# Optimization experiments

Hardware: AMD Instinct MI355X
Metric: run time of the kernel (lower is better)

## Reference

```python
import jax, jax.numpy as jnp
import numpy as np
from jax import lax

N_MAX = 350  # fixed adjacency size from the original module

def _conv(x, w, b):
    y = lax.conv_general_dilated(x, w, (1, 1), 'SAME',
                                 dimension_numbers=('NCHW', 'OIHW', 'NCHW'))
    return y + b[None, :, None, None]

def _maxpool2(x):
    return lax.reduce_window(x, -jnp.inf, lax.max, (1, 1, 2, 2), (1, 1, 2, 2), 'VALID')

def _lin(x, w, b):  # torch Linear: w [out,in]
    return x @ w.T + b

def setup_inputs() -> dict:
    key = jax.random.key(0)
    ks = jax.random.split(key, 24)
    B = 16
    images = jax.random.normal(ks[0], (B, 1, 256, 256), dtype=jnp.float32)
    # prefix masks: first n_b nodes valid, n_b in [2, 350]
    counts = jax.random.randint(ks[1], (B,), 2, N_MAX + 1)
    node_masks = jnp.arange(N_MAX)[None, :] < counts[:, None]
    def p(k, shape, s=0.02):
        return jax.random.normal(k, shape, dtype=jnp.float32) * s
    inp = {
        'images': images, 'node_masks': node_masks,
        # baseline CNN: 1->32->64->128->256, 3x3 convs
        'c1w': p(ks[2], (32, 1, 3, 3)),   'c1b': p(ks[3], (32,)),
        'c2w': p(ks[4], (64, 32, 3, 3)),  'c2b': p(ks[5], (64,)),
        'c3w': p(ks[6], (128, 64, 3, 3)), 'c3b': p(ks[7], (128,)),
        'c4w': p(ks[8], (256, 128, 3, 3)),'c4b': p(ks[9], (256,)),
        # node_detector: 256->512->700
        'nd1w': p(ks[10], (512, 256)), 'nd1b': p(ks[11], (512,)),
        'nd2w': p(ks[12], (N_MAX * 2, 512)), 'nd2b': p(ks[13], (N_MAX * 2,)),
        # count_predictor: 256->256->1
        'cp1w': p(ks[14], (256, 256)), 'cp1b': p(ks[15], (256,)),
        'cp2w': p(ks[16], (1, 256)),   'cp2b': p(ks[17], (1,)),
        # mlp_correction: 1->32->16->1
        'mc1w': p(ks[18], (32, 1)),  'mc1b': p(ks[19], (32,)),
        'mc2w': p(ks[20], (16, 32)), 'mc2b': p(ks[21], (16,)),
        'mc3w': p(ks[22], (1, 16)),  'mc3b': p(ks[23], (1,)),
    }
    return inp

def reference(images, node_masks,
              c1w, c1b, c2w, c2b, c3w, c3b, c4w, c4b,
              nd1w, nd1b, nd2w, nd2b,
              cp1w, cp1b, cp2w, cp2b,
              mc1w, mc1b, mc2w, mc2b, mc3w, mc3b):
    B = images.shape[0]
    relu = jax.nn.relu
    # CNN encoder (baseline)
    x = _maxpool2(relu(_conv(images, c1w, c1b)))
    x = _maxpool2(relu(_conv(x, c2w, c2b)))
    x = _maxpool2(relu(_conv(x, c3w, c3b)))
    x = relu(_conv(x, c4w, c4b))
    feat = jnp.mean(x, axis=(2, 3))  # AdaptiveAvgPool2d((1,1)) -> [B,256]
    # node detector (dropout is identity in eval)
    coords = _lin(relu(_lin(feat, nd1w, nd1b)), nd2w, nd2b).reshape(B, N_MAX, 2)
    # count predictor
    count = _lin(relu(_lin(feat, cp1w, cp1b)), cp2w, cp2b)[:, 0]
    # cosine similarity over all 350 slots (row-wise normalize is mask-independent)
    cn = coords / jnp.maximum(jnp.linalg.norm(coords, axis=-1, keepdims=True), 1e-12)
    sim = jnp.einsum('bnd,bmd->bnm', cn, cn)  # [B,350,350]
    # pointwise 1->32->16->1 MLP correction + sigmoid
    h1 = relu(sim[..., None] * mc1w[:, 0] + mc1b)          # [B,N,N,32]
    h2 = relu(jnp.einsum('bnmk,jk->bnmj', h1, mc2w) + mc2b)  # [B,N,N,16]
    corr = jax.nn.sigmoid(jnp.einsum('bnmj,oj->bnmo', h2, mc3w)[..., 0] + mc3b[0])
    # scatter-pad into fixed 350x350: with prefix masks this is elementwise pair masking
    m = node_masks.astype(corr.dtype)
    pair = m[:, :, None] * m[:, None, :]
    valid = (node_masks.sum(-1) > 1).astype(corr.dtype)  # n_nodes<=1 -> zero adj
    adjacency = corr * pair * valid[:, None, None]
    return (coords, adjacency, count)
```

## Files before the change

kernel.cpp:

```cpp
#include <hip/hip_runtime.h>
#include <hip/hip_bf16.h>
#include <math.h>

typedef __hip_bfloat16 bf16;
typedef __attribute__((ext_vector_type(8))) short short8;
typedef __attribute__((ext_vector_type(4))) float f32x4;

__device__ __forceinline__ bf16 f2b(float v){ return __float2bfloat16(v); }
__device__ __forceinline__ float ldf(float v){ return v; }
__device__ __forceinline__ float ldf(bf16 v){ return __bfloat162float(v); }
__device__ __forceinline__ unsigned short fbits(float v){
  __hip_bfloat16 h = __float2bfloat16(v);
  return *reinterpret_cast<unsigned short*>(&h);
}
__device__ __forceinline__ float dot4(float4 a, float4 b){
  return fmaf(a.x,b.x, fmaf(a.y,b.y, fmaf(a.z,b.z, a.w*b.w)));
}
__device__ __forceinline__ void load_lds16(const bf16* src, void* lds){
  __builtin_amdgcn_global_load_lds(
      (const __attribute__((address_space(1))) void*)src,
      (__attribute__((address_space(3))) void*)lds, 16, 0, 0);
}

__global__ __launch_bounds__(256) void k_c1prep(const float* __restrict__ img,
                        const float* __restrict__ c1w, const float* __restrict__ c1b,
                        bf16* __restrict__ x1,
                        const float* __restrict__ c2w, const float* __restrict__ c3w,
                        const float* __restrict__ c4w, bf16* __restrict__ wt2,
                        bf16* __restrict__ wt3, bf16* __restrict__ wt4,
                        const float* __restrict__ w1, const float* __restrict__ b1,
                        const float* __restrict__ w2, const float* __restrict__ b2,
                        const float* __restrict__ w3, const float* __restrict__ b3,
                        float* __restrict__ lut){
  int bid = blockIdx.x;
  int tid = threadIdx.x;
  if(bid >= 1024){
    int pb = bid - 1024;
    if(pb < 1512){
      int e = pb*256 + tid;
      const float* w; bf16* wt; int OC, IC;
      if(e < 18432){ w = c2w; wt = wt2; OC = 64;  IC = 32; }
      else if(e < 92160){ e -= 18432; w = c3w; wt = wt3; OC = 128; IC = 64; }
      else { e -= 92160; w = c4w; wt = wt4; OC = 256; IC = 128; }
      int ic = e % IC; int t2 = e / IC; int oc = t2 % OC; int tap = t2 / OC;
      wt[e] = f2b(w[(oc*IC + ic)*9 + tap]);
    } else {
      int e = (pb-1512)*256 + tid;
      float s = -1.f + (2.f/4095.f)*e;
      float h1[32];
      #pragma unroll
      for(int k=0;k<32;k++) h1[k] = fmaxf(fmaf(s, w1[k], b1[k]), 0.f);
      float a3 = b3[0];
      #pragma unroll
      for(int j=0;j<16;j++){
        float t = b2[j];
        #pragma unroll
        for(int k=0;k<32;k++) t = fmaf(h1[k], w2[j*32+k], t);
        a3 = fmaf(fmaxf(t,0.f), w3[j], a3);
      }
      lut[e] = 1.f/(1.f + expf(-a3));
    }
    return;
  }
  __shared__ float Wl[288], Bl[32];
  for(int t=tid; t<288; t+=256) Wl[t] = c1w[t];
  if(tid<32) Bl[tid] = c1b[tid];
  __syncthreads();
  int idx = bid*256 + tid;
  int ox = idx & 127, oy = (idx>>7)&127, b = idx>>14;
  const float* ip = img + (size_t)b*65536;
  int y0 = oy*2-1, x0 = ox*2-1;
  float patch[4][4];
  #pragma unroll
  for(int py=0;py<4;py++){
    int y=y0+py; bool yok = (unsigned)y<256u;
    #pragma unroll
    for(int px=0;px<4;px++){
      int x=x0+px;
      patch[py][px] = (yok && (unsigned)x<256u) ? ip[y*256+x] : 0.f;
    }
  }
  unsigned u[16];
  #pragma unroll
  for(int og=0; og<16; og++){
    unsigned short hb[2];
    #pragma unroll
    for(int h=0; h<2; h++){
      int oc = og*2 + h;
      const float* wj = &Wl[oc*9];
      float best = 0.f;
      #pragma unroll
      for(int py=0;py<2;py++)
      #pragma unroll
      for(int px=0;px<2;px++){
        float a = Bl[oc];
        #pragma unroll
        for(int ky=0;ky<3;ky++)
        #pragma unroll
        for(int kx=0;kx<3;kx++)
          a = fmaf(wj[ky*3+kx], patch[py+ky][px+kx], a);
        best = fmaxf(best, a);
      }
      hb[h] = fbits(best);
    }
    u[og] = (unsigned)hb[0] | ((unsigned)hb[1] << 16);
  }
  uint4* dst = (uint4*)(x1 + (size_t)idx*32);
  dst[0] = make_uint4(u[0],u[1],u[2],u[3]);
  dst[1] = make_uint4(u[4],u[5],u[6],u[7]);
  dst[2] = make_uint4(u[8],u[9],u[10],u[11]);
  dst[3] = make_uint4(u[12],u[13],u[14],u[15]);
}

template<int L>
__global__ __launch_bounds__(256) void k_convmfma(const bf16* __restrict__ in,
                      const bf16* __restrict__ wt, const float* __restrict__ bias,
                      bf16* __restrict__ out, float* __restrict__ partial2){
  constexpr int IC   = L==2?32:(L==3?64:128);
  constexpr int OC   = L==2?64:(L==3?128:256);
  constexpr int HW   = L==2?128:(L==3?64:32);
  constexpr int POOL = L==4?0:1;
  constexpr int WNF  = L==4?2:4;
  constexpr int IC8  = IC/8;
  constexpr int SM   = (IC8-1)&7;
  constexpr int KC   = IC/32;
  constexpr int XT   = HW;
  constexpr int ROW  = XT*IC8;
  constexpr int ROWC = (XT+2)*IC8;
  __shared__ short8 T[4*ROWC];

  int bid = blockIdx.x;
  int b, py, bt = 0;
  if(L==4){ b = bid>>5; py = (bid>>1)&15; bt = bid&1; }
  else if(L==3){ b = bid>>5; py = bid&31; }
  else { b = bid>>6; py = bid&63; }

  int tid = threadIdx.x;
  int w = tid>>6, l15 = tid&15, lhi = (tid>>4)&3, lane = tid&63;

  int mbase, nbase;
  if(L==2){ mbase = w*32; nbase = 0; }
  else if(L==3){ mbase = (w&1)*32; nbase = (w>>1)*64; }
  else { mbase = 0; nbase = bt*128 + w*32; }

  for(int c=tid; c<4*2*IC8; c+=256){
    int r = c/(2*IC8), rem = c%(2*IC8);
    int X = (rem>=IC8)?(XT+1):0;
    int k = rem%IC8;
    short8 z = {0,0,0,0,0,0,0,0};
    T[(r*(XT+2)+X)*IC8 + k] = z;
  }
  for(int c0=0; c0<4*ROW; c0+=256){
    int cw  = c0 + w*64;
    int r   = cw / ROW;
    int rem = cw % ROW;
    int gy  = 2*py - 1 + r;
    int ldsbase = (r*(XT+2)+1)*IC8 + rem;
    if((unsigned)gy < (unsigned)HW){
      int remL = rem + lane;
      int x = remL / IC8, k = remL % IC8;
      int ksrc = k ^ ((x+1)&SM);
      const bf16* src = in + (((size_t)b*HW + gy)*XT + x)*IC + ksrc*8;
      load_lds16(src, (void*)&T[ldsbase]);
    } else {
      short8 z = {0,0,0,0,0,0,0,0};
      T[ldsbase + lane] = z;
    }
  }
  __syncthreads();

  float bv[WNF];
  #pragma unroll
  for(int n=0;n<WNF;n++) bv[n] = bias[nbase + n*16 + l15];
  f32x4 acc[2][2][WNF];
  #pragma unroll
  for(int r=0;r<2;r++)
  #pragma unroll
  for(int m=0;m<2;m++)
  #pragma unroll
  for(int n=0;n<WNF;n++){
    acc[r][m][n][0]=bv[n]; acc[r][m][n][1]=bv[n];
    acc[r][m][n][2]=bv[n]; acc[r][m][n][3]=bv[n];
  }

  const short8* wt8 = (const short8*)wt;
  #pragma unroll
  for(int tap=0; tap<9; tap++){
    const int dy = tap/3 - 1, dx = tap%3 - 1;
    #pragma unroll
    for(int kc=0; kc<KC; kc++){
      short8 Bf[WNF];
      #pragma unroll
      for(int n=0;n<WNF;n++){
        int oc = nbase + n*16 + l15;
        Bf[n] = wt8[(size_t)(tap*OC + oc)*IC8 + kc*4 + lhi];
      }
      short8 Af[2][2];
      #pragma unroll
      for(int r=0;r<2;r++)
      #pragma unroll
      for(int m=0;m<2;m++){
        int X = mbase + m*16 + l15 + dx + 1;
        int rs = r + dy + 1;
        Af[r][m] = T[(rs*(XT+2)+X)*IC8 + ((kc*4+lhi) ^ (X&SM))];
      }
      #pragma unroll
      for(int r=0;r<2;r++)
      #pragma unroll
      for(int m=0;m<2;m++)
      #pragma unroll
      for(int n=0;n<WNF;n++)
        acc[r][m][n] = __builtin_amdgcn_mfma_f32_16x16x32_bf16(Af[r][m], Bf[n], acc[r][m][n], 0,0,0);
    }
  }

  if(POOL){
    constexpr int HP = HW/2;
    #pragma unroll
    for(int m=0;m<2;m++)
    #pragma unroll
    for(int n=0;n<WNF;n++){
      int oc = nbase + n*16 + l15;
      #pragma unroll
      for(int t=0;t<2;t++){
        float v = fmaxf(fmaxf(acc[0][m][n][2*t], acc[0][m][n][2*t+1]),
                        fmaxf(acc[1][m][n][2*t], acc[1][m][n][2*t+1]));
        v = fmaxf(v, 0.f);
        int xp = (mbase + m*16)/2 + lhi*2 + t;
        out[(((size_t)b*HP + py)*HP + xp)*OC + oc] = f2b(v);
      }
    }
  } else {
    #pragma unroll
    for(int n=0;n<WNF;n++){
      float p = 0.f;
      #pragma unroll
      for(int r=0;r<2;r++)
      #pragma unroll
      for(int m=0;m<2;m++)
      #pragma unroll
      for(int j=0;j<4;j++)
        p += fmaxf(acc[r][m][n][j], 0.f);
      p += __shfl_xor(p, 16);
      p += __shfl_xor(p, 32);
      if(lhi == 0)
        partial2[((size_t)(b*16+py))*256 + nbase + n*16 + l15] = p;
    }
  }
}

__global__ __launch_bounds__(256) void k_headA(const float* __restrict__ partial2,
                      const float* __restrict__ nd1w, const float* __restrict__ nd1b,
                      const float* __restrict__ cp1w, const float* __restrict__ cp1b,
                      float* __restrict__ h512, float* __restrict__ h256){
  __shared__ float F[256];
  int b = blockIdx.x / 192, blk = blockIdx.x % 192;
  int tid = threadIdx.x;
  float s = 0.f;
  #pragma unroll
  for(int q=0;q<16;q++) s += partial2[((size_t)(b*16+q))*256 + tid];
  F[tid] = s * (1.f/1024.f);
  __syncthreads();
  int w = tid>>6, lane = tid&63;
  int o = blk*4 + w;
  float4 xv = ((const float4*)F)[lane];
  const float* wrow; float bb; float* dst; int oo;
  if(o < 512){ wrow = nd1w + (size_t)o*256; bb = nd1b[o]; dst = h512 + b*512 + o; }
  else { oo = o - 512; wrow = cp1w + (size_t)oo*256; bb = cp1b[oo]; dst = h256 + b*256 + oo; }
  float a = dot4(((const float4*)wrow)[lane], xv);
  #pragma unroll
  for(int off=32; off>0; off>>=1) a += __shfl_xor(a, off);
  if(lane==0) *dst = fmaxf(a + bb, 0.f);
}

__global__ __launch_bounds__(256) void k_headB(const float* __restrict__ h512,
                      const float* __restrict__ h256,
                      const float* __restrict__ nd2w, const float* __restrict__ nd2b,
                      const float* __restrict__ cp2w, const float* __restrict__ cp2b,
                      float* __restrict__ coordsOut, float* __restrict__ countOut){
  int b = blockIdx.x / 176, blk = blockIdx.x % 176;
  int tid = threadIdx.x;
  int w = tid>>6, lane = tid&63;
  int o = blk*4 + w;
  if(o > 700) return;
  float a;
  if(o < 700){
    const float4* xp = (const float4*)(h512 + b*512);
    const float4* wp = (const float4*)(nd2w + (size_t)o*512);
    a = dot4(wp[lane], xp[lane]) + dot4(wp[lane+64], xp[lane+64]);
  } else {
    const float4* xp = (const float4*)(h256 + b*256);
    const float4* wp = (const float4*)cp2w;
    a = dot4(wp[lane], xp[lane]);
  }
  #pragma unroll
  for(int off=32; off>0; off>>=1) a += __shfl_xor(a, off);
  if(lane==0){
    if(o < 700) coordsOut[b*700 + o] = a + nd2b[o];
    else        countOut[b] = a + cp2b[0];
  }
}

__device__ __forceinline__ int mask_mode(const void* p){
  unsigned w0 = ((const unsigned*)p)[0];
  unsigned w1 = ((const unsigned*)p)[1];
  if(w0 == 1u) return (w1 == 0u) ? 4 : 0;
  if(w0 == 0x3F800000u) return 3;
  unsigned short h0 = (unsigned short)(w0 & 0xFFFFu);
  if(h0 == 0x3F80u || h0 == 0x3C00u) return 2;
  return 1;
}
__device__ __forceinline__ int mask_get(const void* p, int i, int mode){
  switch(mode){
    case 0: return ((const int*)p)[i] != 0;
    case 1: return ((const unsigned char*)p)[i] != 0;
    case 2: return ((const unsigned short*)p)[i] != 0;
    case 3: return ((const float*)p)[i] != 0.f;
    default: return ((const long long*)p)[i] != 0ll;
  }
}

__global__ __launch_bounds__(256) void k_adj(const float* __restrict__ coords,
                      const void* __restrict__ masks, const float* __restrict__ lut,
                      float* __restrict__ out){
  int t4 = blockIdx.x*256 + threadIdx.x;
  if(t4 >= 490000) return;
  int base = t4*4;
  int b = base / 122500;
  int rem = base % 122500;
  int mode = mask_mode(masks);
  int valid = mask_get(masks, b*350+1, mode);
  float res[4];
  #pragma unroll
  for(int e=0;e<4;e++){
    int n = (rem+e)/350, m = (rem+e)%350;
    float o = 0.f;
    if(valid && mask_get(masks, b*350+n, mode) && mask_get(masks, b*350+m, mode)){
      float2 a = ((const float2*)coords)[b*350+n];
      float2 c = ((const float2*)coords)[b*350+m];
      float dn = fmaxf(sqrtf(fmaf(a.x,a.x, a.y*a.y)), 1e-12f);
      float dm = fmaxf(sqrtf(fmaf(c.x,c.x, c.y*c.y)), 1e-12f);
      float s = fmaf(a.x, c.x, a.y*c.y) / (dn*dm);
      float u = (s + 1.f) * 2047.5f;
      u = fminf(fmaxf(u, 0.f), 4095.f);
      int i = min((int)u, 4094);
      float fr = u - (float)i;
      float l0 = lut[i], l1 = lut[i+1];
      o = fmaf(l1 - l0, fr, l0);
    }
    res[e] = o;
  }
  *(float4*)(out + base) = make_float4(res[0], res[1], res[2], res[3]);
}

extern "C" void kernel_launch(void* const* d_in, const int* in_sizes, int n_in,
                              void* d_out, int out_size, void* d_ws, size_t ws_size,
                              hipStream_t stream){
  const float* images = (const float*)d_in[0];
  const void*  masks  = d_in[1];
  const float *c1w=(const float*)d_in[2],  *c1b=(const float*)d_in[3];
  const float *c2w=(const float*)d_in[4],  *c2b=(const float*)d_in[5];
  const float *c3w=(const float*)d_in[6],  *c3b=(const float*)d_in[7];
  const float *c4w=(const float*)d_in[8],  *c4b=(const float*)d_in[9];
  const float *nd1w=(const float*)d_in[10],*nd1b=(const float*)d_in[11];
  const float *nd2w=(const float*)d_in[12],*nd2b=(const float*)d_in[13];
  const float *cp1w=(const float*)d_in[14],*cp1b=(const float*)d_in[15];
  const float *cp2w=(const float*)d_in[16],*cp2b=(const float*)d_in[17];
  const float *mc1w=(const float*)d_in[18],*mc1b=(const float*)d_in[19];
  const float *mc2w=(const float*)d_in[20],*mc2b=(const float*)d_in[21];
  const float *mc3w=(const float*)d_in[22],*mc3b=(const float*)d_in[23];
  float* out = (float*)d_out;

  char* W = (char*)d_ws;
  float* partial2 = (float*)W;
  float* h512     = (float*)(W + 262144);
  float* h256     = (float*)(W + 294912);
  float* lut      = (float*)(W + 311296);
  bf16*  wt2 = (bf16*)(W + 524288);
  bf16*  wt3 = (bf16*)(W + 589824);
  bf16*  wt4 = (bf16*)(W + 786432);
  bf16*  x1 = (bf16*)(W + 2097152);
  bf16*  x2 = (bf16*)(W + 2097152 + 16777216);
  bf16*  x3 = (bf16*)(W + 2097152);

  float* coordsOut = out;
  float* adjOut    = out + 11200;
  float* countOut  = out + 11200 + 1960000;

  k_c1prep<<<2552, 256, 0, stream>>>(images, c1w, c1b, x1,
                                     c2w, c3w, c4w, wt2, wt3, wt4,
                                     mc1w, mc1b, mc2w, mc2b, mc3w, mc3b, lut);
  k_convmfma<2><<<1024, 256, 0, stream>>>(x1, wt2, c2b, x2, nullptr);
  k_convmfma<3><<<512, 256, 0, stream>>>(x2, wt3, c3b, x3, nullptr);
  k_convmfma<4><<<512, 256, 0, stream>>>(x3, wt4, c4b, nullptr, partial2);
  k_headA<<<3072, 256, 0, stream>>>(partial2, nd1w, nd1b, cp1w, cp1b, h512, h256);
  k_headB<<<2816, 256, 0, stream>>>(h512, h256, nd2w, nd2b, cp2w, cp2b,
                                    coordsOut, countOut);
  k_adj<<<1915, 256, 0, stream>>>(coordsOut, masks, lut, adjOut);
}
```

Measured before the change: 95.57 us.

## Split conv4 over input channels and precompute mask counts for adjacency

Conv4 is split into two input-channel halves across twice as many blocks, each writing raw per-pixel partial sums to a large workspace. The head kernel then combines the halves, applies ReLU and averages over all pixels. Mask counts are computed once in the second head kernel so the adjacency kernel can use prefix comparisons. The split adds a large global write and a heavy redundant re-read in every head block.

```diff
diff --git a/kernel.cpp b/kernel.cpp
--- a/kernel.cpp
+++ b/kernel.cpp
@@ -122,16 +122,16 @@
   constexpr int POOL = L==4?0:1;
   constexpr int WNF  = L==4?2:4;
   constexpr int IC8  = IC/8;
-  constexpr int SM   = (IC8-1)&7;
-  constexpr int KC   = IC/32;
+  constexpr int IC8S = L==4?8:IC8;
+  constexpr int SMS  = (IC8S-1)&7;
+  constexpr int KCS  = L==4?2:IC/32;
   constexpr int XT   = HW;
-  constexpr int ROW  = XT*IC8;
-  constexpr int ROWC = (XT+2)*IC8;
-  __shared__ short8 T[4*ROWC];
+  constexpr int ROW  = XT*IC8S;
+  __shared__ short8 T[4*(XT+2)*IC8S];
 
   int bid = blockIdx.x;
-  int b, py, bt = 0;
-  if(L==4){ b = bid>>5; py = (bid>>1)&15; bt = bid&1; }
+  int b, py, bt = 0, kq = 0;
+  if(L==4){ b = bid>>6; py = (bid>>2)&15; bt = (bid>>1)&1; kq = bid&1; }
   else if(L==3){ b = bid>>5; py = bid&31; }
   else { b = bid>>6; py = bid&63; }
 
@@ -143,23 +143,23 @@
   else if(L==3){ mbase = (w&1)*32; nbase = (w>>1)*64; }
   else { mbase = 0; nbase = bt*128 + w*32; }
 
-  for(int c=tid; c<4*2*IC8; c+=256){
-    int r = c/(2*IC8), rem = c%(2*IC8);
-    int X = (rem>=IC8)?(XT+1):0;
-    int k = rem%IC8;
+  for(int c=tid; c<4*2*IC8S; c+=256){
+    int r = c/(2*IC8S), rem = c%(2*IC8S);
+    int X = (rem>=IC8S)?(XT+1):0;
+    int k = rem%IC8S;
     short8 z = {0,0,0,0,0,0,0,0};
-    T[(r*(XT+2)+X)*IC8 + k] = z;
+    T[(r*(XT+2)+X)*IC8S + k] = z;
   }
   for(int c0=0; c0<4*ROW; c0+=256){
     int cw  = c0 + w*64;
     int r   = cw / ROW;
     int rem = cw % ROW;
     int gy  = 2*py - 1 + r;
-    int ldsbase = (r*(XT+2)+1)*IC8 + rem;
+    int ldsbase = (r*(XT+2)+1)*IC8S + rem;
     if((unsigned)gy < (unsigned)HW){
       int remL = rem + lane;
-      int x = remL / IC8, k = remL % IC8;
-      int ksrc = k ^ ((x+1)&SM);
+      int x = remL / IC8S, k = remL % IC8S;
+      int ksrc = (k ^ ((x+1)&SMS)) + (L==4 ? kq*8 : 0);
       const bf16* src = in + (((size_t)b*HW + gy)*XT + x)*IC + ksrc*8;
       load_lds16(src, (void*)&T[ldsbase]);
     } else {
@@ -171,7 +171,8 @@
 
   float bv[WNF];
   #pragma unroll
-  for(int n=0;n<WNF;n++) bv[n] = bias[nbase + n*16 + l15];
+  for(int n=0;n<WNF;n++)
+    bv[n] = (L==4 && kq==1) ? 0.f : bias[nbase + n*16 + l15];
   f32x4 acc[2][2][WNF];
   #pragma unroll
   for(int r=0;r<2;r++)
@@ -188,12 +189,12 @@
   for(int tap=0; tap<9; tap++){
     const int dy = tap/3 - 1, dx = tap%3 - 1;
     #pragma unroll
-    for(int kc=0; kc<KC; kc++){
+    for(int kc=0; kc<KCS; kc++){
       short8 Bf[WNF];
       #pragma unroll
       for(int n=0;n<WNF;n++){
         int oc = nbase + n*16 + l15;
-        Bf[n] = wt8[(size_t)(tap*OC + oc)*IC8 + kc*4 + lhi];
+        Bf[n] = wt8[(size_t)(tap*OC + oc)*IC8 + (L==4 ? kq*8 : 0) + kc*4 + lhi];
       }
       short8 Af[2][2];
       #pragma unroll
@@ -202,7 +203,7 @@
       for(int m=0;m<2;m++){
         int X = mbase + m*16 + l15 + dx + 1;
         int rs = r + dy + 1;
-        Af[r][m] = T[(rs*(XT+2)+X)*IC8 + ((kc*4+lhi) ^ (X&SM))];
+        Af[r][m] = T[(rs*(XT+2)+X)*IC8S + ((kc*4+lhi) ^ (X&SMS))];
       }
       #pragma unroll
       for(int r=0;r<2;r++)
@@ -233,32 +234,48 @@
   } else {
     #pragma unroll
     for(int n=0;n<WNF;n++){
-      float p = 0.f;
-      #pragma unroll
-      for(int r=0;r<2;r++)
-      #pragma unroll
-      for(int m=0;m<2;m++)
-      #pragma unroll
-      for(int j=0;j<4;j++)
-        p += fmaxf(acc[r][m][n][j], 0.f);
-      p += __shfl_xor(p, 16);
-      p += __shfl_xor(p, 32);
-      if(lhi == 0)
-        partial2[((size_t)(b*16+py))*256 + nbase + n*16 + l15] = p;
-    }
-  }
-}
-
-__global__ __launch_bounds__(256) void k_headA(const float* __restrict__ partial2,
+      float p[2];
+      #pragma unroll
+      for(int mm=0;mm<2;mm++){
+        float s = 0.f;
+        #pragma unroll
+        for(int r=0;r<2;r++)
+        #pragma unroll
+        for(int j=0;j<4;j++)
+          s += acc[r][mm][n][j];
+        p[mm] = s;
+      }
+      (void)p;
+    }
+    #pragma unroll
+    for(int r=0;r<2;r++)
+    #pragma unroll
+    for(int m=0;m<2;m++)
+    #pragma unroll
+    for(int n=0;n<WNF;n++){
+      int oc = nbase + n*16 + l15;
+      #pragma unroll
+      for(int j=0;j<4;j++){
+        int x = m*16 + lhi*4 + j;
+        partial2[(((((size_t)kq*16 + b)*16 + py)*2 + r)*32 + x)*256 + oc] = acc[r][m][n][j];
+      }
+    }
+  }
+}
+
+__global__ __launch_bounds__(256) void k_headA(const float* __restrict__ pixraw,
                       const float* __restrict__ nd1w, const float* __restrict__ nd1b,
                       const float* __restrict__ cp1w, const float* __restrict__ cp1b,
                       float* __restrict__ h512, float* __restrict__ h256){
   __shared__ float F[256];
   int b = blockIdx.x / 192, blk = blockIdx.x % 192;
   int tid = threadIdx.x;
+  const size_t half = (size_t)16*16*2*32*256;
   float s = 0.f;
-  #pragma unroll
-  for(int q=0;q<16;q++) s += partial2[((size_t)(b*16+q))*256 + tid];
+  for(int pix=0; pix<1024; pix++){
+    size_t idx = (((size_t)b*16 + (pix>>6))*2 + ((pix>>5)&1))*32*256 + (pix&31)*256 + tid;
+    s += fmaxf(pixraw[idx] + pixraw[half + idx], 0.f);
+  }
   F[tid] = s * (1.f/1024.f);
   __syncthreads();
   int w = tid>>6, lane = tid&63;
@@ -273,15 +290,45 @@
   if(lane==0) *dst = fmaxf(a + bb, 0.f);
 }
 
+__device__ __forceinline__ int mask_mode(const void* p){
+  unsigned w0 = ((const unsigned*)p)[0];
+  unsigned w1 = ((const unsigned*)p)[1];
+  if(w0 == 1u) return (w1 == 0u) ? 4 : 0;
+  if(w0 == 0x3F800000u) return 3;
+  unsigned short h0 = (unsigned short)(w0 & 0xFFFFu);
+  if(h0 == 0x3F80u || h0 == 0x3C00u) return 2;
+  return 1;
+}
+__device__ __forceinline__ int mask_get(const void* p, int i, int mode){
+  switch(mode){
+    case 0: return ((const int*)p)[i] != 0;
+    case 1: return ((const unsigned char*)p)[i] != 0;
+    case 2: return ((const unsigned short*)p)[i] != 0;
+    case 3: return ((const float*)p)[i] != 0.f;
+    default: return ((const long long*)p)[i] != 0ll;
+  }
+}
+
 __global__ __launch_bounds__(256) void k_headB(const float* __restrict__ h512,
                       const float* __restrict__ h256,
                       const float* __restrict__ nd2w, const float* __restrict__ nd2b,
                       const float* __restrict__ cp2w, const float* __restrict__ cp2b,
-                      float* __restrict__ coordsOut, float* __restrict__ countOut){
+                      const void* __restrict__ masks,
+                      float* __restrict__ coordsOut, float* __restrict__ countOut,
+                      int* __restrict__ counts){
   int b = blockIdx.x / 176, blk = blockIdx.x % 176;
   int tid = threadIdx.x;
   int w = tid>>6, lane = tid&63;
   int o = blk*4 + w;
+  if(o == 701){
+    int mode = mask_mode(masks);
+    int c = 0;
+    for(int i=lane; i<350; i+=64) c += mask_get(masks, b*350+i, mode);
+    #pragma unroll
+    for(int off=32; off>0; off>>=1) c += __shfl_xor(c, off);
+    if(lane==0) counts[b] = c;
+    return;
+  }
   if(o > 700) return;
   float a;
   if(o < 700){
@@ -301,41 +348,22 @@
   }
 }
 
-__device__ __forceinline__ int mask_mode(const void* p){
-  unsigned w0 = ((const unsigned*)p)[0];
-  unsigned w1 = ((const unsigned*)p)[1];
-  if(w0 == 1u) return (w1 == 0u) ? 4 : 0;
-  if(w0 == 0x3F800000u) return 3;
-  unsigned short h0 = (unsigned short)(w0 & 0xFFFFu);
-  if(h0 == 0x3F80u || h0 == 0x3C00u) return 2;
-  return 1;
-}
-__device__ __forceinline__ int mask_get(const void* p, int i, int mode){
-  switch(mode){
-    case 0: return ((const int*)p)[i] != 0;
-    case 1: return ((const unsigned char*)p)[i] != 0;
-    case 2: return ((const unsigned short*)p)[i] != 0;
-    case 3: return ((const float*)p)[i] != 0.f;
-    default: return ((const long long*)p)[i] != 0ll;
-  }
-}
-
 __global__ __launch_bounds__(256) void k_adj(const float* __restrict__ coords,
-                      const void* __restrict__ masks, const float* __restrict__ lut,
+                      const int* __restrict__ counts, const float* __restrict__ lut,
                       float* __restrict__ out){
   int t4 = blockIdx.x*256 + threadIdx.x;
   if(t4 >= 490000) return;
   int base = t4*4;
   int b = base / 122500;
   int rem = base % 122500;
-  int mode = mask_mode(masks);
-  int valid = mask_get(masks, b*350+1, mode);
+  int cnt = counts[b];
+  int valid = cnt > 1;
   float res[4];
   #pragma unroll
   for(int e=0;e<4;e++){
     int n = (rem+e)/350, m = (rem+e)%350;
     float o = 0.f;
-    if(valid && mask_get(masks, b*350+n, mode) && mask_get(masks, b*350+m, mode)){
+    if(valid && n < cnt && m < cnt){
       float2 a = ((const float2*)coords)[b*350+n];
       float2 c = ((const float2*)coords)[b*350+m];
       float dn = fmaxf(sqrtf(fmaf(a.x,a.x, a.y*a.y)), 1e-12f);
@@ -372,16 +400,17 @@
   float* out = (float*)d_out;
 
   char* W = (char*)d_ws;
-  float* partial2 = (float*)W;
-  float* h512     = (float*)(W + 262144);
-  float* h256     = (float*)(W + 294912);
-  float* lut      = (float*)(W + 311296);
-  bf16*  wt2 = (bf16*)(W + 524288);
-  bf16*  wt3 = (bf16*)(W + 589824);
-  bf16*  wt4 = (bf16*)(W + 786432);
-  bf16*  x1 = (bf16*)(W + 2097152);
-  bf16*  x2 = (bf16*)(W + 2097152 + 16777216);
-  bf16*  x3 = (bf16*)(W + 2097152);
+  float* pixraw  = (float*)W;
+  float* h512    = (float*)(W + 33554432);
+  float* h256    = (float*)(W + 33587200);
+  float* lut     = (float*)(W + 33603584);
+  int*   counts  = (int*)(W + 33619968);
+  bf16*  wt2 = (bf16*)(W + 33685504);
+  bf16*  wt3 = (bf16*)(W + 33751040);
+  bf16*  wt4 = (bf16*)(W + 33947648);
+  bf16*  x1 = (bf16*)(W + 35651584);
+  bf16*  x2 = (bf16*)(W + 35651584 + 16777216);
+  bf16*  x3 = (bf16*)(W + 35651584);
 
   float* coordsOut = out;
   float* adjOut    = out + 11200;
@@ -392,9 +421,9 @@
                                      mc1w, mc1b, mc2w, mc2b, mc3w, mc3b, lut);
   k_convmfma<2><<<1024, 256, 0, stream>>>(x1, wt2, c2b, x2, nullptr);
   k_convmfma<3><<<512, 256, 0, stream>>>(x2, wt3, c3b, x3, nullptr);
-  k_convmfma<4><<<512, 256, 0, stream>>>(x3, wt4, c4b, nullptr, partial2);
-  k_headA<<<3072, 256, 0, stream>>>(partial2, nd1w, nd1b, cp1w, cp1b, h512, h256);
-  k_headB<<<2816, 256, 0, stream>>>(h512, h256, nd2w, nd2b, cp2w, cp2b,
-                                    coordsOut, countOut);
-  k_adj<<<1915, 256, 0, stream>>>(coordsOut, masks, lut, adjOut);
-}
+  k_convmfma<4><<<1024, 256, 0, stream>>>(x3, wt4, c4b, nullptr, pixraw);
+  k_headA<<<3072, 256, 0, stream>>>(pixraw, nd1w, nd1b, cp1w, cp1b, h512, h256);
+  k_headB<<<2816, 256, 0, stream>>>(h512, h256, nd2w, nd2b, cp2w, cp2b, masks,
+                                    coordsOut, countOut, counts);
+  k_adj<<<1915, 256, 0, stream>>>(coordsOut, counts, lut, adjOut);
+}
```

New measurement: 309.0 us. 223% more time.
